# Optimization experiments

Measured on AMD Instinct MI355X. Metric: run time of the kernel, lower is better.

## Reference

```python
import jax, jax.numpy as jnp
from jax import lax
import numpy as np

B, S, D = 64, 512, 256
VOCAB, NC = 50000, 10
N_STEPS = 10  # ode_step=11 points -> 10 intervals, h=0.1
BN_EPS = 1e-5


def setup_inputs() -> dict:
    key = jax.random.key(0)
    ks = jax.random.split(key, 16)
    inp = {}
    inp['input_ids'] = jax.random.randint(ks[0], (B, S), 0, VOCAB)
    inp['emb'] = jax.random.normal(ks[1], (VOCAB, D), dtype=jnp.float32)
    inp['W_ode'] = 0.1 * jax.random.normal(ks[2], (D, D), dtype=jnp.float32)  # init std=0.1
    inp['b_ode'] = jnp.zeros((D,), dtype=jnp.float32)
    for i, kk in enumerate([3, 4, 5]):
        fan_in = D * kk
        inp[f'w{kk}'] = jax.random.normal(ks[3 + 3 * i], (128, D, kk), jnp.float32) / np.sqrt(fan_in)
        inp[f'b{kk}'] = jax.random.normal(ks[4 + 3 * i], (128,), jnp.float32) * 0.01
        inp[f'g{kk}'] = jnp.ones((128,), jnp.float32)
        inp[f'be{kk}'] = jnp.zeros((128,), jnp.float32)
    inp['wc'] = jax.random.normal(ks[12], (NC, D + 3 * 128), jnp.float32) / np.sqrt(D + 3 * 128)
    inp['bc'] = jnp.zeros((NC,), jnp.float32)
    return inp


def _forward(input_ids, emb, W_ode, b_ode, w3, b3, g3, be3, w4, b4, g4, be4,
             w5, b5, g5, be5, wc, bc):
    x = emb[input_ids]                      # (B,S,D)
    # --- Neural ODE branch: linear RHS f(z) = z W^T + b, RK4 fixed-step on [0,1] ---
    z0 = x.reshape(-1, D)                   # (B*S, D)
    h = jnp.float32(1.0 / N_STEPS)

    def f(z):
        return z @ W_ode.T + b_ode

    def step(z, _):
        k1 = f(z)
        k2 = f(z + 0.5 * h * k1)
        k3 = f(z + 0.5 * h * k2)
        k4 = f(z + h * k3)
        return z + (h / 6.0) * (k1 + 2 * k2 + 2 * k3 + k4), None

    z, _ = lax.scan(step, z0, None, length=N_STEPS)
    node_pooled = z.reshape(B, S, D).max(axis=1)   # global max over seq -> (B,D)

    # --- TextCNN branches on raw embeddings ---
    cin = jnp.transpose(x, (0, 2, 1))       # (B,D,S)
    inv_std = jnp.float32(1.0 / np.sqrt(1.0 + BN_EPS))  # BN eval: mean=0, var=1

    def branch(w, b, g, be):
        c = lax.conv_general_dilated(cin, w, (1,), 'VALID',
                                     dimension_numbers=('NCH', 'OIH', 'NCH'))
        c = c + b[None, :, None]
        c = g[None, :, None] * (c * inv_std) + be[None, :, None]
        c = jax.nn.relu(c)
        return c.max(axis=2)                # (B,128)

    p3 = branch(w3, b3, g3, be3)
    p4 = branch(w4, b4, g4, be4)
    p5 = branch(w5, b5, g5, be5)

    feats = jnp.concatenate([node_pooled, p3, p4, p5], axis=1)  # (B,640)
    return feats @ wc.T + bc                # (B,NC); dropout is identity in eval


def reference(input_ids, emb, W_ode, b_ode, w3, b3, g3, be3, w4, b4, g4, be4,
              w5, b5, g5, be5, wc, bc):
    return _forward(input_ids, emb, W_ode, b_ode, w3, b3, g3, be3,
                    w4, b4, g4, be4, w5, b5, g5, be5, wc, bc)
```

## Files before the change

kernel.cpp:

```cpp
#include <hip/hip_runtime.h>


typedef short bf16x8 __attribute__((ext_vector_type(8)));
typedef float f32x4 __attribute__((ext_vector_type(4)));

__device__ __forceinline__ unsigned short f2bf(float f) {
  unsigned u = __float_as_uint(f);
  u += 0x7FFFu + ((u >> 16) & 1u);
  return (unsigned short)(u >> 16);
}

__device__ __forceinline__ float dotcol(const float* __restrict__ xrow,
                                        const float* __restrict__ Y, int tid) {
  float a0 = 0.f, a1 = 0.f, a2 = 0.f, a3 = 0.f;
#pragma unroll 4
  for (int k = 0; k < 256; k += 16) {
    float bv[16];
#pragma unroll
    for (int u = 0; u < 16; ++u) bv[u] = Y[(k + u) * 256 + tid];
#pragma unroll
    for (int u = 0; u < 16; u += 4) {
      a0 = fmaf(xrow[k + u + 0], bv[u + 0], a0);
      a1 = fmaf(xrow[k + u + 1], bv[u + 1], a1);
      a2 = fmaf(xrow[k + u + 2], bv[u + 2], a2);
      a3 = fmaf(xrow[k + u + 3], bv[u + 3], a3);
    }
  }
  return (a0 + a1) + (a2 + a3);
}

__device__ __forceinline__ float rowscan(const float* __restrict__ cvec,
                                         const float* __restrict__ row, float init) {
  float a0 = init, a1 = 0.f, a2 = 0.f, a3 = 0.f;
#pragma unroll 4
  for (int k = 0; k < 256; k += 16) {
    float bv[16];
#pragma unroll
    for (int u = 0; u < 16; ++u) bv[u] = row[k + u];
#pragma unroll
    for (int u = 0; u < 16; u += 4) {
      a0 = fmaf(cvec[k + u + 0], bv[u + 0], a0);
      a1 = fmaf(cvec[k + u + 1], bv[u + 1], a1);
      a2 = fmaf(cvec[k + u + 2], bv[u + 2], a2);
      a3 = fmaf(cvec[k + u + 3], bv[u + 3], a3);
    }
  }
  return (a0 + a1) + (a2 + a3);
}

__global__ __launch_bounds__(256) void k_prep1(
    const float* __restrict__ W, const float* __restrict__ bode,
    const float* __restrict__ w3, const float* __restrict__ w4c, const float* __restrict__ w5,
    float* __restrict__ B, float* __restrict__ c1,
    unsigned short* __restrict__ slab, unsigned* __restrict__ featbuf) {
  __shared__ float r1[256], r2[256], r3[256], red[4];
  const int tid = threadIdx.x, blk = blockIdx.x;
  if (blk < 256) {
    const int i = blk;
    r1[tid] = W[i * 256 + tid];
    __syncthreads();
    const float v2 = dotcol(r1, W, tid);
    r2[tid] = v2;
    __syncthreads();
    const float v3 = dotcol(r2, W, tid);
    r3[tid] = v3;
    __syncthreads();
    const float v4 = dotcol(r3, W, tid);
    const float w1 = r1[tid];
    B[i * 256 + tid] = 0.1f * w1 + 0.005f * v2
                     + (0.001f / 6.f) * v3 + (0.0001f / 24.f) * v4;
    const float q = 0.05f * w1 + (0.01f / 6.f) * v2 + (0.001f / 24.f) * v3;
    float val = bode[tid] * q;
#pragma unroll
    for (int off = 32; off > 0; off >>= 1) val += __shfl_down(val, off);
    if ((tid & 63) == 0) red[tid >> 6] = val;
    __syncthreads();
    if (tid == 0) c1[i] = 0.1f * (bode[i] + ((red[0] + red[1]) + (red[2] + red[3])));
  } else {
    const int base = (blk - 256) * 256 + tid;
#pragma unroll
    for (int u = 0; u < 4; ++u) {
      int e = base + u * 98304;
      int s = e >> 15, r = e & 32767, kd = r >> 7, o = r & 127;
      const float* w; int k, j;
      if (s < 3)      { w = w3;  k = 3; j = s; }
      else if (s < 7) { w = w4c; k = 4; j = s - 3; }
      else            { w = w5;  k = 5; j = s - 7; }
      float val = w[(o * 256 + kd) * k + j];
      int kc = kd >> 5, quad = (kd >> 3) & 3, q8 = kd & 7;
      slab[s * 32768 + ((kc * 4 + quad) * 128 + o) * 8 + q8] = f2bf(val);
    }
    if (base < 64 * 640) featbuf[base] = 0u;
  }
}

__global__ __launch_bounds__(256) void k_prep2(const float* __restrict__ B,
                                               float* __restrict__ N2) {
  __shared__ float xrow[256];
  const int tid = threadIdx.x, i = blockIdx.x;
  xrow[tid] = B[i * 256 + tid];
  __syncthreads();
  const float s = dotcol(xrow, B, tid);
  N2[i * 256 + tid] = ((i == tid) ? 1.f : 0.f) + 2.f * xrow[tid] + s;
}

__global__ __launch_bounds__(256) void k_prep3(
    const float* __restrict__ B, const float* __restrict__ N2,
    const float* __restrict__ c1, float* __restrict__ c10,
    unsigned short* __restrict__ slab) {
  __shared__ float xr[256], c2s[256];
  const int tid = threadIdx.x, blk = blockIdx.x;
  if (blk < 256) {
    xr[tid] = N2[blk * 256 + tid];
    __syncthreads();
    float v = 0.f;
#pragma unroll 1
    for (int it = 0; it < 4; ++it) {
      v = dotcol(xr, N2, tid);
      __syncthreads();
      xr[tid] = v;
      __syncthreads();
    }
    const int o = blk, kd = tid;
    const int kc = kd >> 5, quad = (kd >> 3) & 3, q8 = kd & 7;
    slab[(12 + (o >> 7)) * 32768 + ((kc * 4 + quad) * 128 + (o & 127)) * 8 + q8] = f2bf(v);
  } else {
    const int j = tid;
    xr[tid] = c1[tid];
    __syncthreads();
    float acc = rowscan(xr, B + (size_t)j * 256, 2.f * xr[j]);
    __syncthreads();
    xr[j] = acc; c2s[j] = acc;
    __syncthreads();
#pragma unroll 1
    for (int it = 0; it < 4; ++it) {
      float a = rowscan(xr, N2 + (size_t)j * 256, c2s[j]);
      __syncthreads();
      xr[j] = a;
      __syncthreads();
    }
    c10[j] = xr[j];
  }
}


__global__ __launch_bounds__(256, 2) void k_main(
    const int* __restrict__ ids, const float* __restrict__ emb,
    const unsigned short* __restrict__ slab, const float* __restrict__ ctot,
    const float* __restrict__ b3, const float* __restrict__ g3, const float* __restrict__ be3,
    const float* __restrict__ b4, const float* __restrict__ g4, const float* __restrict__ be4,
    const float* __restrict__ b5, const float* __restrict__ g5, const float* __restrict__ be5,
    unsigned* __restrict__ featbuf) {
  __shared__ alignas(16) unsigned short Xt[68 * 264];
  __shared__ int ids_s[68];
  const int tid = threadIdx.x;
  const int blk = blockIdx.x;
  const int b = blk >> 3;
  const int t0 = (blk & 7) * 64;
  const int lane = tid & 63;
  const int wave = tid >> 6;
  const int m15 = lane & 15;
  const int quad = lane >> 4;

  if (tid < 68) {
    int t = t0 + tid;
    ids_s[tid] = (t < 512) ? ids[b * 512 + t] : -1;
  }
  __syncthreads();
  for (int i = tid; i < 68 * 64; i += 256) {
    int row = i >> 6, s4 = i & 63;
    uint2 v = make_uint2(0u, 0u);
    int id = ids_s[row];
    if (id >= 0) {
      const float4 f = *(const float4*)(emb + (size_t)id * 256 + s4 * 4);
      v.x = (unsigned)f2bf(f.x) | ((unsigned)f2bf(f.y) << 16);
      v.y = (unsigned)f2bf(f.z) | ((unsigned)f2bf(f.w) << 16);
    }
    *(uint2*)&Xt[row * 264 + s4 * 4] = v;
  }
  __syncthreads();

  const unsigned short* fb0 = slab + ((size_t)quad * 128 + (wave * 2 + 0) * 16 + m15) * 8;
  const unsigned short* fb1 = fb0 + 128;

  bf16x8 fA[4], fB[4];
#pragma unroll
  for (int q = 0; q < 4; ++q) {
    fA[q] = *(const bf16x8*)(((q & 1) ? fb1 : fb0) + (q >> 1) * 4096);
    fB[q] = *(const bf16x8*)(((q & 1) ? fb1 : fb0) + 8192 + (q >> 1) * 4096);
  }

  f32x4 acc[4][2];
#pragma unroll
  for (int mt = 0; mt < 4; ++mt)
#pragma unroll
    for (int nt = 0; nt < 2; ++nt) acc[mt][nt] = (f32x4){0.f, 0.f, 0.f, 0.f};

#define ENTRY(KCQ, FR)                                                          \
  {                                                                             \
    _Pragma("unroll")                                                           \
    for (int kc2 = 0; kc2 < 2; ++kc2) {                                         \
      const int kd0 = ((KCQ) * 2 + kc2) * 32 + quad * 8;                        \
      bf16x8 af[4];                                                             \
      _Pragma("unroll")                                                         \
      for (int mt = 0; mt < 4; ++mt)                                            \
        af[mt] = *(const bf16x8*)&Xt[(shift + mt * 16 + m15) * 264 + kd0];      \
      _Pragma("unroll")                                                         \
      for (int mt = 0; mt < 4; ++mt) {                                          \
        acc[mt][0] = __builtin_amdgcn_mfma_f32_16x16x32_bf16(af[mt], FR[kc2 * 2 + 0], acc[mt][0], 0, 0, 0); \
        acc[mt][1] = __builtin_amdgcn_mfma_f32_16x16x32_bf16(af[mt], FR[kc2 * 2 + 1], acc[mt][1], 0, 0, 0); \
      }                                                                         \
    }                                                                           \
  }

  for (int ep = 0; ep < 28; ++ep) {
    const int e0 = ep * 2;
    const int slice = e0 >> 2;
    const int shift = (slice < 3) ? slice
                    : (slice < 7) ? (slice - 3)
                    : (slice < 12) ? (slice - 7) : 0;
    const int kcq0 = e0 & 3;

    ENTRY(kcq0, fA);
    if (ep < 27) {
      const int eo = (e0 + 2) * 8192;
#pragma unroll
      for (int q = 0; q < 4; ++q)
        fA[q] = *(const bf16x8*)(((q & 1) ? fb1 : fb0) + eo + (q >> 1) * 4096);
    }
    ENTRY(kcq0 + 1, fB);
    if (ep < 27) {
      const int eo = (e0 + 3) * 8192;
#pragma unroll
      for (int q = 0; q < 4; ++q)
        fB[q] = *(const bf16x8*)(((q & 1) ? fb1 : fb0) + eo + (q >> 1) * 4096);
    }

    const int g = (ep == 5) ? 0 : (ep == 13) ? 1 : (ep == 23) ? 2
                : (ep == 25) ? 3 : (ep == 27) ? 4 : -1;
    if (g >= 0) {
      if (g < 3) {
        const int kk = g + 3;
        const float* bb  = (g == 0) ? b3 : (g == 1) ? b4 : b5;
        const float* gg  = (g == 0) ? g3 : (g == 1) ? g4 : g5;
        const float* bbe = (g == 0) ? be3 : (g == 1) ? be4 : be5;
        const int off = 256 + g * 128;
        const int tmax = 512 - kk;
#pragma unroll
        for (int nt = 0; nt < 2; ++nt) {
          const int n = (wave * 2 + nt) * 16 + m15;
          const float sc = gg[n] * 0.9999950000375f;
          const float sh = fmaf(sc, bb[n], bbe[n]);
          float mx = 0.f;
#pragma unroll
          for (int mt = 0; mt < 4; ++mt)
#pragma unroll
            for (int r = 0; r < 4; ++r) {
              const int t = t0 + mt * 16 + quad * 4 + r;
              const float v = fmaf(sc, acc[mt][nt][r], sh);
              if (t <= tmax) mx = fmaxf(mx, v);
            }
          mx = fmaxf(mx, __shfl_xor(mx, 16));
          mx = fmaxf(mx, __shfl_xor(mx, 32));
          if (quad == 0) atomicMax(&featbuf[b * 640 + off + n], __float_as_uint(mx));
        }
      } else {
        const int base = (g == 3) ? 0 : 128;
#pragma unroll
        for (int nt = 0; nt < 2; ++nt) {
          const int n = (wave * 2 + nt) * 16 + m15;
          const float ct = ctot[base + n];
          float mx = -3.4e38f;
#pragma unroll
          for (int mt = 0; mt < 4; ++mt)
#pragma unroll
            for (int r = 0; r < 4; ++r)
              mx = fmaxf(mx, acc[mt][nt][r] + ct);
          mx = fmaxf(mx, __shfl_xor(mx, 16));
          mx = fmaxf(mx, __shfl_xor(mx, 32));
          if (quad == 0) {
            unsigned bits = __float_as_uint(mx);
            unsigned key = (bits & 0x80000000u) ? ~bits : (bits | 0x80000000u);
            atomicMax(&featbuf[b * 640 + base + n], key);
          }
        }
      }
#pragma unroll
      for (int mt = 0; mt < 4; ++mt)
#pragma unroll
        for (int nt = 0; nt < 2; ++nt) acc[mt][nt] = (f32x4){0.f, 0.f, 0.f, 0.f};
    }
  }
#undef ENTRY
}

__global__ void k_fin(const unsigned* __restrict__ featbuf, const float* __restrict__ wc,
                      const float* __restrict__ bc, float* __restrict__ out) {
  int b = blockIdx.x, lane = threadIdx.x;
  float p[10];
#pragma unroll
  for (int c = 0; c < 10; ++c) p[c] = 0.f;
  for (int f = lane; f < 640; f += 64) {
    unsigned u = featbuf[b * 640 + f];
    float v;
    if (f < 256) v = (u & 0x80000000u) ? __uint_as_float(u ^ 0x80000000u) : __uint_as_float(~u);
    else v = __uint_as_float(u);
#pragma unroll
    for (int c = 0; c < 10; ++c) p[c] = fmaf(v, wc[c * 640 + f], p[c]);
  }
#pragma unroll
  for (int c = 0; c < 10; ++c) {
    float s = p[c];
#pragma unroll
    for (int off = 32; off > 0; off >>= 1) s += __shfl_down(s, off);
    if (lane == 0) out[b * 10 + c] = s + bc[c];
  }
}

extern "C" void kernel_launch(void* const* d_in, const int* in_sizes, int n_in,
                              void* d_out, int out_size, void* d_ws, size_t ws_size,
                              hipStream_t stream) {
  (void)in_sizes; (void)n_in; (void)out_size; (void)ws_size;
  const int*   ids  = (const int*)d_in[0];
  const float* emb  = (const float*)d_in[1];
  const float* W    = (const float*)d_in[2];
  const float* bode = (const float*)d_in[3];
  const float* w3   = (const float*)d_in[4];
  const float* b3   = (const float*)d_in[5];
  const float* g3   = (const float*)d_in[6];
  const float* be3  = (const float*)d_in[7];
  const float* w4   = (const float*)d_in[8];
  const float* b4   = (const float*)d_in[9];
  const float* g4   = (const float*)d_in[10];
  const float* be4  = (const float*)d_in[11];
  const float* w5   = (const float*)d_in[12];
  const float* b5   = (const float*)d_in[13];
  const float* g5   = (const float*)d_in[14];
  const float* be5  = (const float*)d_in[15];
  const float* wc   = (const float*)d_in[16];
  const float* bc   = (const float*)d_in[17];
  float* out = (float*)d_out;

  float* wsf = (float*)d_ws;
  float* B   = wsf;
  float* N2  = wsf + 65536;
  float* c1  = wsf + 131072;
  float* c10 = wsf + 131328;
  unsigned short* slab = (unsigned short*)(wsf + 131584);
  unsigned* featbuf = (unsigned*)(wsf + 360960);

  hipLaunchKernelGGL(k_prep1, dim3(640), dim3(256), 0, stream,
                     W, bode, w3, w4, w5, B, c1, slab, featbuf);
  hipLaunchKernelGGL(k_prep2, dim3(256), dim3(256), 0, stream, B, N2);
  hipLaunchKernelGGL(k_prep3, dim3(257), dim3(256), 0, stream, B, N2, c1, c10, slab);
  hipLaunchKernelGGL(k_main, dim3(512), dim3(256), 0, stream,
                     ids, emb, slab, c10,
                     b3, g3, be3, b4, g4, be4, b5, g5, be5, featbuf);
  hipLaunchKernelGGL(k_fin, dim3(64), dim3(64), 0, stream, featbuf, wc, bc, out);
}
```

Baseline: 223.2 us.

## Fuse all stages into one persistent kernel with software grid barriers

Merges the three prep kernels, the main conv/ODE kernel and the classifier into a single 512-block launch, separating stages with an atomic-counter grid barrier instead of kernel boundaries. The main loop now keeps four bf16 fragment sets in flight instead of two and issues the fragment loads before the embedding gather. The aim is to remove launch gaps and tail idle time between the five kernels. The risks are a hang if all 512 blocks cannot be co-resident (it relies on 2 blocks per CU), the cost of spinning blocks at each barrier, higher register pressure, and an extra memset launch.

```diff
diff --git a/kernel.cpp b/kernel.cpp
--- a/kernel.cpp
+++ b/kernel.cpp
@@ -48,113 +48,130 @@
   return (a0 + a1) + (a2 + a3);
 }
 
-__global__ __launch_bounds__(256) void k_prep1(
+__device__ __forceinline__ void gbar(unsigned* __restrict__ cnt,
+                                     unsigned* __restrict__ flag) {
+  __syncthreads();
+  if (threadIdx.x == 0) {
+    __threadfence();
+    unsigned my = __hip_atomic_load(flag, __ATOMIC_RELAXED, __HIP_MEMORY_SCOPE_AGENT);
+    if (atomicAdd(cnt, 1u) == 511u) {
+      __hip_atomic_store(cnt, 0u, __ATOMIC_RELAXED, __HIP_MEMORY_SCOPE_AGENT);
+      __hip_atomic_store(flag, my + 1u, __ATOMIC_RELEASE, __HIP_MEMORY_SCOPE_AGENT);
+    } else {
+      while (__hip_atomic_load(flag, __ATOMIC_RELAXED, __HIP_MEMORY_SCOPE_AGENT) == my)
+        __builtin_amdgcn_s_sleep(2);
+    }
+    __threadfence();
+  }
+  __syncthreads();
+}
+
+__global__ __launch_bounds__(256, 2) void k_mega(
+    const int* __restrict__ ids, const float* __restrict__ emb,
     const float* __restrict__ W, const float* __restrict__ bode,
-    const float* __restrict__ w3, const float* __restrict__ w4c, const float* __restrict__ w5,
-    float* __restrict__ B, float* __restrict__ c1,
-    unsigned short* __restrict__ slab, unsigned* __restrict__ featbuf) {
-  __shared__ float r1[256], r2[256], r3[256], red[4];
-  const int tid = threadIdx.x, blk = blockIdx.x;
-  if (blk < 256) {
-    const int i = blk;
-    r1[tid] = W[i * 256 + tid];
-    __syncthreads();
-    const float v2 = dotcol(r1, W, tid);
-    r2[tid] = v2;
-    __syncthreads();
-    const float v3 = dotcol(r2, W, tid);
-    r3[tid] = v3;
-    __syncthreads();
-    const float v4 = dotcol(r3, W, tid);
-    const float w1 = r1[tid];
-    B[i * 256 + tid] = 0.1f * w1 + 0.005f * v2
-                     + (0.001f / 6.f) * v3 + (0.0001f / 24.f) * v4;
-    const float q = 0.05f * w1 + (0.01f / 6.f) * v2 + (0.001f / 24.f) * v3;
-    float val = bode[tid] * q;
-#pragma unroll
-    for (int off = 32; off > 0; off >>= 1) val += __shfl_down(val, off);
-    if ((tid & 63) == 0) red[tid >> 6] = val;
-    __syncthreads();
-    if (tid == 0) c1[i] = 0.1f * (bode[i] + ((red[0] + red[1]) + (red[2] + red[3])));
-  } else {
-    const int base = (blk - 256) * 256 + tid;
-#pragma unroll
-    for (int u = 0; u < 4; ++u) {
-      int e = base + u * 98304;
-      int s = e >> 15, r = e & 32767, kd = r >> 7, o = r & 127;
-      const float* w; int k, j;
-      if (s < 3)      { w = w3;  k = 3; j = s; }
-      else if (s < 7) { w = w4c; k = 4; j = s - 3; }
-      else            { w = w5;  k = 5; j = s - 7; }
-      float val = w[(o * 256 + kd) * k + j];
-      int kc = kd >> 5, quad = (kd >> 3) & 3, q8 = kd & 7;
-      slab[s * 32768 + ((kc * 4 + quad) * 128 + o) * 8 + q8] = f2bf(val);
-    }
-    if (base < 64 * 640) featbuf[base] = 0u;
-  }
-}
-
-__global__ __launch_bounds__(256) void k_prep2(const float* __restrict__ B,
-                                               float* __restrict__ N2) {
-  __shared__ float xrow[256];
-  const int tid = threadIdx.x, i = blockIdx.x;
-  xrow[tid] = B[i * 256 + tid];
-  __syncthreads();
-  const float s = dotcol(xrow, B, tid);
-  N2[i * 256 + tid] = ((i == tid) ? 1.f : 0.f) + 2.f * xrow[tid] + s;
-}
-
-__global__ __launch_bounds__(256) void k_prep3(
-    const float* __restrict__ B, const float* __restrict__ N2,
-    const float* __restrict__ c1, float* __restrict__ c10,
-    unsigned short* __restrict__ slab) {
-  __shared__ float xr[256], c2s[256];
-  const int tid = threadIdx.x, blk = blockIdx.x;
-  if (blk < 256) {
-    xr[tid] = N2[blk * 256 + tid];
-    __syncthreads();
-    float v = 0.f;
-#pragma unroll 1
-    for (int it = 0; it < 4; ++it) {
-      v = dotcol(xr, N2, tid);
-      __syncthreads();
-      xr[tid] = v;
-      __syncthreads();
-    }
-    const int o = blk, kd = tid;
-    const int kc = kd >> 5, quad = (kd >> 3) & 3, q8 = kd & 7;
-    slab[(12 + (o >> 7)) * 32768 + ((kc * 4 + quad) * 128 + (o & 127)) * 8 + q8] = f2bf(v);
-  } else {
-    const int j = tid;
-    xr[tid] = c1[tid];
-    __syncthreads();
-    float acc = rowscan(xr, B + (size_t)j * 256, 2.f * xr[j]);
-    __syncthreads();
-    xr[j] = acc; c2s[j] = acc;
-    __syncthreads();
-#pragma unroll 1
-    for (int it = 0; it < 4; ++it) {
-      float a = rowscan(xr, N2 + (size_t)j * 256, c2s[j]);
-      __syncthreads();
-      xr[j] = a;
-      __syncthreads();
-    }
-    c10[j] = xr[j];
-  }
-}
-
-
-__global__ __launch_bounds__(256, 2) void k_main(
-    const int* __restrict__ ids, const float* __restrict__ emb,
-    const unsigned short* __restrict__ slab, const float* __restrict__ ctot,
-    const float* __restrict__ b3, const float* __restrict__ g3, const float* __restrict__ be3,
-    const float* __restrict__ b4, const float* __restrict__ g4, const float* __restrict__ be4,
-    const float* __restrict__ b5, const float* __restrict__ g5, const float* __restrict__ be5,
-    unsigned* __restrict__ featbuf) {
+    const float* __restrict__ w3c, const float* __restrict__ b3,
+    const float* __restrict__ g3, const float* __restrict__ be3,
+    const float* __restrict__ w4c, const float* __restrict__ b4,
+    const float* __restrict__ g4, const float* __restrict__ be4,
+    const float* __restrict__ w5c, const float* __restrict__ b5,
+    const float* __restrict__ g5, const float* __restrict__ be5,
+    const float* __restrict__ wc, const float* __restrict__ bc,
+    float* __restrict__ out,
+    float* __restrict__ Bm, float* __restrict__ N2,
+    float* __restrict__ c1, float* __restrict__ c10,
+    unsigned short* __restrict__ slab, unsigned* __restrict__ featbuf,
+    unsigned* __restrict__ bar) {
   __shared__ alignas(16) unsigned short Xt[68 * 264];
   __shared__ int ids_s[68];
   const int tid = threadIdx.x;
   const int blk = blockIdx.x;
+
+  float* r1  = (float*)Xt;
+  float* r2  = r1 + 256;
+  float* r3  = r1 + 512;
+  float* red = r1 + 768;
+
+  if (blk < 256) {
+    const int i = blk;
+    r1[tid] = W[i * 256 + tid];
+    __syncthreads();
+    const float v2 = dotcol(r1, W, tid);
+    r2[tid] = v2;
+    __syncthreads();
+    const float v3 = dotcol(r2, W, tid);
+    r3[tid] = v3;
+    __syncthreads();
+    const float v4 = dotcol(r3, W, tid);
+    const float w1 = r1[tid];
+    Bm[i * 256 + tid] = 0.1f * w1 + 0.005f * v2
+                      + (0.001f / 6.f) * v3 + (0.0001f / 24.f) * v4;
+    const float q = 0.05f * w1 + (0.01f / 6.f) * v2 + (0.001f / 24.f) * v3;
+    float val = bode[tid] * q;
+#pragma unroll
+    for (int off = 32; off > 0; off >>= 1) val += __shfl_down(val, off);
+    if ((tid & 63) == 0) red[tid >> 6] = val;
+    __syncthreads();
+    if (tid == 0) c1[i] = 0.1f * (bode[i] + ((red[0] + red[1]) + (red[2] + red[3])));
+  } else {
+    const int base = (blk - 256) * 256 + tid;
+#pragma unroll
+    for (int u = 0; u < 6; ++u) {
+      int e = base + u * 65536;
+      int s = e >> 15, r = e & 32767, kd = r >> 7, o = r & 127;
+      const float* w; int k, j;
+      if (s < 3)      { w = w3c; k = 3; j = s; }
+      else if (s < 7) { w = w4c; k = 4; j = s - 3; }
+      else            { w = w5c; k = 5; j = s - 7; }
+      float val = w[(o * 256 + kd) * k + j];
+      int kc = kd >> 5, quad = (kd >> 3) & 3, q8 = kd & 7;
+      slab[s * 32768 + ((kc * 4 + quad) * 128 + o) * 8 + q8] = f2bf(val);
+    }
+    if (base < 64 * 640) featbuf[base] = 0u;
+  }
+  gbar(bar, bar + 1);
+
+  if (blk < 256) {
+    r1[tid] = Bm[blk * 256 + tid];
+    __syncthreads();
+    const float s = dotcol(r1, Bm, tid);
+    N2[blk * 256 + tid] = ((blk == tid) ? 1.f : 0.f) + 2.f * r1[tid] + s;
+  } else if (blk == 300) {
+    r1[tid] = c1[tid];
+    __syncthreads();
+    const float acc = rowscan(r1, Bm + (size_t)tid * 256, 2.f * r1[tid]);
+    __syncthreads();
+    r1[tid] = acc;
+    r2[tid] = acc;
+    __syncthreads();
+  }
+  gbar(bar, bar + 1);
+
+  if (blk < 256) {
+    r1[tid] = N2[blk * 256 + tid];
+    __syncthreads();
+    float v = 0.f;
+#pragma unroll 1
+    for (int it = 0; it < 4; ++it) {
+      v = dotcol(r1, N2, tid);
+      __syncthreads();
+      r1[tid] = v;
+      __syncthreads();
+    }
+    const int o = blk, kd = tid;
+    const int kc = kd >> 5, quad = (kd >> 3) & 3, q8 = kd & 7;
+    slab[(12 + (o >> 7)) * 32768 + ((kc * 4 + quad) * 128 + (o & 127)) * 8 + q8] = f2bf(v);
+  } else if (blk == 300) {
+#pragma unroll 1
+    for (int it = 0; it < 4; ++it) {
+      const float a = rowscan(r1, N2 + (size_t)tid * 256, r2[tid]);
+      __syncthreads();
+      r1[tid] = a;
+      __syncthreads();
+    }
+    c10[tid] = r1[tid];
+  }
+  gbar(bar, bar + 1);
+
   const int b = blk >> 3;
   const int t0 = (blk & 7) * 64;
   const int lane = tid & 63;
@@ -167,6 +184,19 @@
     ids_s[tid] = (t < 512) ? ids[b * 512 + t] : -1;
   }
   __syncthreads();
+
+  const unsigned short* fb0 = slab + ((size_t)quad * 128 + wave * 2 * 16 + m15) * 8;
+  bf16x8 fA[4], fB[4], fC[4], fD[4];
+#define LDFRAG(DST, EN)                                                         \
+  {                                                                             \
+    const unsigned short* p_ = fb0 + (EN) * 8192;                               \
+    DST[0] = *(const bf16x8*)(p_);                                              \
+    DST[1] = *(const bf16x8*)(p_ + 128);                                        \
+    DST[2] = *(const bf16x8*)(p_ + 4096);                                       \
+    DST[3] = *(const bf16x8*)(p_ + 4096 + 128);                                 \
+  }
+  LDFRAG(fA, 0) LDFRAG(fB, 1) LDFRAG(fC, 2) LDFRAG(fD, 3)
+
   for (int i = tid; i < 68 * 64; i += 256) {
     int row = i >> 6, s4 = i & 63;
     uint2 v = make_uint2(0u, 0u);
@@ -179,16 +209,6 @@
     *(uint2*)&Xt[row * 264 + s4 * 4] = v;
   }
   __syncthreads();
-
-  const unsigned short* fb0 = slab + ((size_t)quad * 128 + (wave * 2 + 0) * 16 + m15) * 8;
-  const unsigned short* fb1 = fb0 + 128;
-
-  bf16x8 fA[4], fB[4];
-#pragma unroll
-  for (int q = 0; q < 4; ++q) {
-    fA[q] = *(const bf16x8*)(((q & 1) ? fb1 : fb0) + (q >> 1) * 4096);
-    fB[q] = *(const bf16x8*)(((q & 1) ? fb1 : fb0) + 8192 + (q >> 1) * 4096);
-  }
 
   f32x4 acc[4][2];
 #pragma unroll
@@ -213,31 +233,16 @@
     }                                                                           \
   }
 
-  for (int ep = 0; ep < 28; ++ep) {
-    const int e0 = ep * 2;
-    const int slice = e0 >> 2;
-    const int shift = (slice < 3) ? slice
-                    : (slice < 7) ? (slice - 3)
-                    : (slice < 12) ? (slice - 7) : 0;
-    const int kcq0 = e0 & 3;
-
-    ENTRY(kcq0, fA);
-    if (ep < 27) {
-      const int eo = (e0 + 2) * 8192;
-#pragma unroll
-      for (int q = 0; q < 4; ++q)
-        fA[q] = *(const bf16x8*)(((q & 1) ? fb1 : fb0) + eo + (q >> 1) * 4096);
-    }
-    ENTRY(kcq0 + 1, fB);
-    if (ep < 27) {
-      const int eo = (e0 + 3) * 8192;
-#pragma unroll
-      for (int q = 0; q < 4; ++q)
-        fB[q] = *(const bf16x8*)(((q & 1) ? fb1 : fb0) + eo + (q >> 1) * 4096);
-    }
-
-    const int g = (ep == 5) ? 0 : (ep == 13) ? 1 : (ep == 23) ? 2
-                : (ep == 25) ? 3 : (ep == 27) ? 4 : -1;
+  for (int eq = 0; eq < 14; ++eq) {
+    const int shift = (eq < 3) ? eq : (eq < 7) ? (eq - 3) : (eq < 12) ? (eq - 7) : 0;
+
+    ENTRY(0, fA) if (eq < 13) LDFRAG(fA, (eq + 1) * 4 + 0)
+    ENTRY(1, fB) if (eq < 13) LDFRAG(fB, (eq + 1) * 4 + 1)
+    ENTRY(2, fC) if (eq < 13) LDFRAG(fC, (eq + 1) * 4 + 2)
+    ENTRY(3, fD) if (eq < 13) LDFRAG(fD, (eq + 1) * 4 + 3)
+
+    const int g = (eq == 2) ? 0 : (eq == 6) ? 1 : (eq == 11) ? 2
+                : (eq == 12) ? 3 : (eq == 13) ? 4 : -1;
     if (g >= 0) {
       if (g < 3) {
         const int kk = g + 3;
@@ -269,7 +274,7 @@
 #pragma unroll
         for (int nt = 0; nt < 2; ++nt) {
           const int n = (wave * 2 + nt) * 16 + m15;
-          const float ct = ctot[base + n];
+          const float ct = c10[base + n];
           float mx = -3.4e38f;
 #pragma unroll
           for (int mt = 0; mt < 4; ++mt)
@@ -292,28 +297,35 @@
     }
   }
 #undef ENTRY
-}
-
-__global__ void k_fin(const unsigned* __restrict__ featbuf, const float* __restrict__ wc,
-                      const float* __restrict__ bc, float* __restrict__ out) {
-  int b = blockIdx.x, lane = threadIdx.x;
-  float p[10];
-#pragma unroll
-  for (int c = 0; c < 10; ++c) p[c] = 0.f;
-  for (int f = lane; f < 640; f += 64) {
-    unsigned u = featbuf[b * 640 + f];
-    float v;
-    if (f < 256) v = (u & 0x80000000u) ? __uint_as_float(u ^ 0x80000000u) : __uint_as_float(~u);
-    else v = __uint_as_float(u);
-#pragma unroll
-    for (int c = 0; c < 10; ++c) p[c] = fmaf(v, wc[c * 640 + f], p[c]);
-  }
-#pragma unroll
-  for (int c = 0; c < 10; ++c) {
-    float s = p[c];
-#pragma unroll
-    for (int off = 32; off > 0; off >>= 1) s += __shfl_down(s, off);
-    if (lane == 0) out[b * 10 + c] = s + bc[c];
+#undef LDFRAG
+
+  gbar(bar, bar + 1);
+  if (blk < 64 && tid < 64) {
+    float vv[10];
+#pragma unroll
+    for (int it = 0; it < 10; ++it) {
+      unsigned u = featbuf[blk * 640 + it * 64 + tid];
+      if (it < 4)
+        vv[it] = (u & 0x80000000u) ? __uint_as_float(u ^ 0x80000000u)
+                                   : __uint_as_float(~u);
+      else
+        vv[it] = __uint_as_float(u);
+    }
+    float p[10];
+#pragma unroll
+    for (int c = 0; c < 10; ++c) p[c] = 0.f;
+#pragma unroll
+    for (int it = 0; it < 10; ++it)
+#pragma unroll
+      for (int c = 0; c < 10; ++c)
+        p[c] = fmaf(vv[it], wc[c * 640 + it * 64 + tid], p[c]);
+#pragma unroll
+    for (int c = 0; c < 10; ++c) {
+      float s = p[c];
+#pragma unroll
+      for (int off = 32; off > 0; off >>= 1) s += __shfl_down(s, off);
+      if (tid == 0) out[blk * 10 + c] = s + bc[c];
+    }
   }
 }
 
@@ -342,19 +354,17 @@
   float* out = (float*)d_out;
 
   float* wsf = (float*)d_ws;
-  float* B   = wsf;
+  float* Bm  = wsf;
   float* N2  = wsf + 65536;
   float* c1  = wsf + 131072;
   float* c10 = wsf + 131328;
   unsigned short* slab = (unsigned short*)(wsf + 131584);
   unsigned* featbuf = (unsigned*)(wsf + 360960);
-
-  hipLaunchKernelGGL(k_prep1, dim3(640), dim3(256), 0, stream,
-                     W, bode, w3, w4, w5, B, c1, slab, featbuf);
-  hipLaunchKernelGGL(k_prep2, dim3(256), dim3(256), 0, stream, B, N2);
-  hipLaunchKernelGGL(k_prep3, dim3(257), dim3(256), 0, stream, B, N2, c1, c10, slab);
-  hipLaunchKernelGGL(k_main, dim3(512), dim3(256), 0, stream,
-                     ids, emb, slab, c10,
-                     b3, g3, be3, b4, g4, be4, b5, g5, be5, featbuf);
-  hipLaunchKernelGGL(k_fin, dim3(64), dim3(64), 0, stream, featbuf, wc, bc, out);
-}
+  unsigned* bar     = (unsigned*)(wsf + 401920);
+
+  hipMemsetAsync(bar, 0, 8, stream);
+  hipLaunchKernelGGL(k_mega, dim3(512), dim3(256), 0, stream,
+                     ids, emb, W, bode,
+                     w3, b3, g3, be3, w4, b4, g4, be4, w5, b5, g5, be5,
+                     wc, bc, out, Bm, N2, c1, c10, slab, featbuf, bar);
+}
```

After: 426.2 us. 1.91x slower.

## Split prep matrix-vector steps across 1024 threads and deepen main fragment prefetch

Applied to the files above, without the earlier changes.

The prep kernels go from 256 to 1024 threads per block. Each row-times-matrix step is split into four K-partitions whose partial sums are reduced through shared memory, and the c-vector recurrence now uses wave-per-row shuffle reductions instead of serial row scans. This is meant to cut the latency of the serial chains of dot products in the prep stage. In the main kernel, weight fragments are now double-buffered four entries deep and loaded before the embedding gather, so more global loads are in flight. That raises register pressure under the existing occupancy-2 launch bound.

```diff
diff --git a/kernel.cpp b/kernel.cpp
--- a/kernel.cpp
+++ b/kernel.cpp
@@ -10,82 +10,67 @@
   return (unsigned short)(u >> 16);
 }
 
-__device__ __forceinline__ float dotcol(const float* __restrict__ xrow,
-                                        const float* __restrict__ Y, int tid) {
+__device__ __forceinline__ void rstep(float* __restrict__ dst, const float* __restrict__ src,
+                                      const float* __restrict__ Y, float* __restrict__ part,
+                                      int t) {
+  const int c = t & 255, g = t >> 8;
+  const float* Yc = Y + (size_t)(g * 64) * 256 + c;
+  const float* sg = src + g * 64;
   float a0 = 0.f, a1 = 0.f, a2 = 0.f, a3 = 0.f;
 #pragma unroll 4
-  for (int k = 0; k < 256; k += 16) {
+  for (int u = 0; u < 64; u += 16) {
     float bv[16];
 #pragma unroll
-    for (int u = 0; u < 16; ++u) bv[u] = Y[(k + u) * 256 + tid];
-#pragma unroll
-    for (int u = 0; u < 16; u += 4) {
-      a0 = fmaf(xrow[k + u + 0], bv[u + 0], a0);
-      a1 = fmaf(xrow[k + u + 1], bv[u + 1], a1);
-      a2 = fmaf(xrow[k + u + 2], bv[u + 2], a2);
-      a3 = fmaf(xrow[k + u + 3], bv[u + 3], a3);
-    }
-  }
-  return (a0 + a1) + (a2 + a3);
-}
-
-__device__ __forceinline__ float rowscan(const float* __restrict__ cvec,
-                                         const float* __restrict__ row, float init) {
-  float a0 = init, a1 = 0.f, a2 = 0.f, a3 = 0.f;
-#pragma unroll 4
-  for (int k = 0; k < 256; k += 16) {
-    float bv[16];
-#pragma unroll
-    for (int u = 0; u < 16; ++u) bv[u] = row[k + u];
-#pragma unroll
-    for (int u = 0; u < 16; u += 4) {
-      a0 = fmaf(cvec[k + u + 0], bv[u + 0], a0);
-      a1 = fmaf(cvec[k + u + 1], bv[u + 1], a1);
-      a2 = fmaf(cvec[k + u + 2], bv[u + 2], a2);
-      a3 = fmaf(cvec[k + u + 3], bv[u + 3], a3);
-    }
-  }
-  return (a0 + a1) + (a2 + a3);
-}
-
-__global__ __launch_bounds__(256) void k_prep1(
+    for (int v = 0; v < 16; ++v) bv[v] = Yc[(u + v) * 256];
+#pragma unroll
+    for (int v = 0; v < 16; v += 4) {
+      a0 = fmaf(sg[u + v + 0], bv[v + 0], a0);
+      a1 = fmaf(sg[u + v + 1], bv[v + 1], a1);
+      a2 = fmaf(sg[u + v + 2], bv[v + 2], a2);
+      a3 = fmaf(sg[u + v + 3], bv[v + 3], a3);
+    }
+  }
+  part[t] = (a0 + a1) + (a2 + a3);
+  __syncthreads();
+  if (t < 256) dst[t] = (part[t] + part[t + 256]) + (part[t + 512] + part[t + 768]);
+  __syncthreads();
+}
+
+__global__ __launch_bounds__(1024) void k_prep1(
     const float* __restrict__ W, const float* __restrict__ bode,
-    const float* __restrict__ w3, const float* __restrict__ w4c, const float* __restrict__ w5,
-    float* __restrict__ B, float* __restrict__ c1,
+    const float* __restrict__ w3c, const float* __restrict__ w4c, const float* __restrict__ w5c,
+    float* __restrict__ Bm, float* __restrict__ c1,
     unsigned short* __restrict__ slab, unsigned* __restrict__ featbuf) {
-  __shared__ float r1[256], r2[256], r3[256], red[4];
-  const int tid = threadIdx.x, blk = blockIdx.x;
+  __shared__ float part[1024], ra[256], rb[256], rc[256], rd[256], red[4];
+  const int t = threadIdx.x, blk = blockIdx.x;
   if (blk < 256) {
     const int i = blk;
-    r1[tid] = W[i * 256 + tid];
+    if (t < 256) ra[t] = W[i * 256 + t];
     __syncthreads();
-    const float v2 = dotcol(r1, W, tid);
-    r2[tid] = v2;
+    rstep(rb, ra, W, part, t);
+    rstep(rc, rb, W, part, t);
+    rstep(rd, rc, W, part, t);
+    if (t < 256) {
+      Bm[i * 256 + t] = 0.1f * ra[t] + 0.005f * rb[t]
+                      + (0.001f / 6.f) * rc[t] + (0.0001f / 24.f) * rd[t];
+      const float q = 0.05f * ra[t] + (0.01f / 6.f) * rb[t] + (0.001f / 24.f) * rc[t];
+      float val = bode[t] * q;
+#pragma unroll
+      for (int off = 32; off > 0; off >>= 1) val += __shfl_down(val, off);
+      if ((t & 63) == 0) red[t >> 6] = val;
+    }
     __syncthreads();
-    const float v3 = dotcol(r2, W, tid);
-    r3[tid] = v3;
-    __syncthreads();
-    const float v4 = dotcol(r3, W, tid);
-    const float w1 = r1[tid];
-    B[i * 256 + tid] = 0.1f * w1 + 0.005f * v2
-                     + (0.001f / 6.f) * v3 + (0.0001f / 24.f) * v4;
-    const float q = 0.05f * w1 + (0.01f / 6.f) * v2 + (0.001f / 24.f) * v3;
-    float val = bode[tid] * q;
-#pragma unroll
-    for (int off = 32; off > 0; off >>= 1) val += __shfl_down(val, off);
-    if ((tid & 63) == 0) red[tid >> 6] = val;
-    __syncthreads();
-    if (tid == 0) c1[i] = 0.1f * (bode[i] + ((red[0] + red[1]) + (red[2] + red[3])));
+    if (t == 0) c1[i] = 0.1f * (bode[i] + ((red[0] + red[1]) + (red[2] + red[3])));
   } else {
-    const int base = (blk - 256) * 256 + tid;
+    const int base = (blk - 256) * 1024 + t;
 #pragma unroll
     for (int u = 0; u < 4; ++u) {
       int e = base + u * 98304;
       int s = e >> 15, r = e & 32767, kd = r >> 7, o = r & 127;
       const float* w; int k, j;
-      if (s < 3)      { w = w3;  k = 3; j = s; }
+      if (s < 3)      { w = w3c; k = 3; j = s; }
       else if (s < 7) { w = w4c; k = 4; j = s - 3; }
-      else            { w = w5;  k = 5; j = s - 7; }
+      else            { w = w5c; k = 5; j = s - 7; }
       float val = w[(o * 256 + kd) * k + j];
       int kc = kd >> 5, quad = (kd >> 3) & 3, q8 = kd & 7;
       slab[s * 32768 + ((kc * 4 + quad) * 128 + o) * 8 + q8] = f2bf(val);
@@ -94,52 +79,68 @@
   }
 }
 
-__global__ __launch_bounds__(256) void k_prep2(const float* __restrict__ B,
-                                               float* __restrict__ N2) {
-  __shared__ float xrow[256];
-  const int tid = threadIdx.x, i = blockIdx.x;
-  xrow[tid] = B[i * 256 + tid];
-  __syncthreads();
-  const float s = dotcol(xrow, B, tid);
-  N2[i * 256 + tid] = ((i == tid) ? 1.f : 0.f) + 2.f * xrow[tid] + s;
-}
-
-__global__ __launch_bounds__(256) void k_prep3(
-    const float* __restrict__ B, const float* __restrict__ N2,
+__global__ __launch_bounds__(1024) void k_prep2(const float* __restrict__ Bm,
+                                                float* __restrict__ N2) {
+  __shared__ float part[1024], ra[256], rb[256];
+  const int t = threadIdx.x, i = blockIdx.x;
+  if (t < 256) ra[t] = Bm[i * 256 + t];
+  __syncthreads();
+  rstep(rb, ra, Bm, part, t);
+  if (t < 256) N2[i * 256 + t] = ((i == t) ? 1.f : 0.f) + 2.f * ra[t] + rb[t];
+}
+
+__global__ __launch_bounds__(1024) void k_prep3(
+    const float* __restrict__ Bm, const float* __restrict__ N2,
     const float* __restrict__ c1, float* __restrict__ c10,
     unsigned short* __restrict__ slab) {
-  __shared__ float xr[256], c2s[256];
-  const int tid = threadIdx.x, blk = blockIdx.x;
+  __shared__ float part[1024], ra[256], rb[256], rc[256], rd[256];
+  const int t = threadIdx.x, blk = blockIdx.x;
   if (blk < 256) {
-    xr[tid] = N2[blk * 256 + tid];
+    if (t < 256) ra[t] = N2[blk * 256 + t];
     __syncthreads();
-    float v = 0.f;
-#pragma unroll 1
-    for (int it = 0; it < 4; ++it) {
-      v = dotcol(xr, N2, tid);
-      __syncthreads();
-      xr[tid] = v;
-      __syncthreads();
-    }
-    const int o = blk, kd = tid;
-    const int kc = kd >> 5, quad = (kd >> 3) & 3, q8 = kd & 7;
-    slab[(12 + (o >> 7)) * 32768 + ((kc * 4 + quad) * 128 + (o & 127)) * 8 + q8] = f2bf(v);
+    rstep(ra, ra, N2, part, t);
+    rstep(ra, ra, N2, part, t);
+    rstep(ra, ra, N2, part, t);
+    rstep(ra, ra, N2, part, t);
+    if (t < 256) {
+      const int o = blk, kd = t;
+      const int kc = kd >> 5, quad = (kd >> 3) & 3, q8 = kd & 7;
+      slab[(12 + (o >> 7)) * 32768 + ((kc * 4 + quad) * 128 + (o & 127)) * 8 + q8] = f2bf(ra[t]);
+    }
   } else {
-    const int j = tid;
-    xr[tid] = c1[tid];
+    const int w = t >> 6, lane = t & 63;
+    if (t < 256) { ra[t] = c1[t]; rd[t] = 2.f * c1[t]; }
     __syncthreads();
-    float acc = rowscan(xr, B + (size_t)j * 256, 2.f * xr[j]);
-    __syncthreads();
-    xr[j] = acc; c2s[j] = acc;
-    __syncthreads();
-#pragma unroll 1
-    for (int it = 0; it < 4; ++it) {
-      float a = rowscan(xr, N2 + (size_t)j * 256, c2s[j]);
-      __syncthreads();
-      xr[j] = a;
-      __syncthreads();
-    }
-    c10[j] = xr[j];
+#define CSTEP(SRC, YMAT, ADD2, DST)                                             \
+    {                                                                           \
+      for (int r0i = 0; r0i < 16; r0i += 4) {                                   \
+        float bv[4][4];                                                         \
+        _Pragma("unroll")                                                       \
+        for (int rr = 0; rr < 4; ++rr) {                                        \
+          const int j = w * 16 + r0i + rr;                                      \
+          _Pragma("unroll")                                                     \
+          for (int q = 0; q < 4; ++q) bv[rr][q] = YMAT[j * 256 + lane + 64 * q];\
+        }                                                                       \
+        _Pragma("unroll")                                                       \
+        for (int rr = 0; rr < 4; ++rr) {                                        \
+          const int j = w * 16 + r0i + rr;                                      \
+          float v = 0.f;                                                        \
+          _Pragma("unroll")                                                     \
+          for (int q = 0; q < 4; ++q) v = fmaf(SRC[lane + 64 * q], bv[rr][q], v);\
+          _Pragma("unroll")                                                     \
+          for (int off = 32; off > 0; off >>= 1) v += __shfl_down(v, off);      \
+          if (lane == 0) DST[j] = ADD2[j] + v;                                  \
+        }                                                                       \
+      }                                                                         \
+      __syncthreads();                                                          \
+    }
+    CSTEP(ra, Bm, rd, rb)
+    CSTEP(rb, N2, rb, rc)
+    CSTEP(rc, N2, rb, rd)
+    CSTEP(rd, N2, rb, rc)
+    CSTEP(rc, N2, rb, rd)
+#undef CSTEP
+    if (t < 256) c10[t] = rd[t];
   }
 }
 
@@ -167,6 +168,19 @@
     ids_s[tid] = (t < 512) ? ids[b * 512 + t] : -1;
   }
   __syncthreads();
+
+  const unsigned short* fb0 = slab + ((size_t)quad * 128 + wave * 2 * 16 + m15) * 8;
+  bf16x8 fA[4], fB[4], fC[4], fD[4];
+#define LDFRAG(DST, EN)                                                         \
+  {                                                                             \
+    const unsigned short* p_ = fb0 + (EN) * 8192;                               \
+    DST[0] = *(const bf16x8*)(p_);                                              \
+    DST[1] = *(const bf16x8*)(p_ + 128);                                        \
+    DST[2] = *(const bf16x8*)(p_ + 4096);                                       \
+    DST[3] = *(const bf16x8*)(p_ + 4096 + 128);                                 \
+  }
+  LDFRAG(fA, 0) LDFRAG(fB, 1) LDFRAG(fC, 2) LDFRAG(fD, 3)
+
   for (int i = tid; i < 68 * 64; i += 256) {
     int row = i >> 6, s4 = i & 63;
     uint2 v = make_uint2(0u, 0u);
@@ -179,16 +193,6 @@
     *(uint2*)&Xt[row * 264 + s4 * 4] = v;
   }
   __syncthreads();
-
-  const unsigned short* fb0 = slab + ((size_t)quad * 128 + (wave * 2 + 0) * 16 + m15) * 8;
-  const unsigned short* fb1 = fb0 + 128;
-
-  bf16x8 fA[4], fB[4];
-#pragma unroll
-  for (int q = 0; q < 4; ++q) {
-    fA[q] = *(const bf16x8*)(((q & 1) ? fb1 : fb0) + (q >> 1) * 4096);
-    fB[q] = *(const bf16x8*)(((q & 1) ? fb1 : fb0) + 8192 + (q >> 1) * 4096);
-  }
 
   f32x4 acc[4][2];
 #pragma unroll
@@ -213,31 +217,16 @@
     }                                                                           \
   }
 
-  for (int ep = 0; ep < 28; ++ep) {
-    const int e0 = ep * 2;
-    const int slice = e0 >> 2;
-    const int shift = (slice < 3) ? slice
-                    : (slice < 7) ? (slice - 3)
-                    : (slice < 12) ? (slice - 7) : 0;
-    const int kcq0 = e0 & 3;
-
-    ENTRY(kcq0, fA);
-    if (ep < 27) {
-      const int eo = (e0 + 2) * 8192;
-#pragma unroll
-      for (int q = 0; q < 4; ++q)
-        fA[q] = *(const bf16x8*)(((q & 1) ? fb1 : fb0) + eo + (q >> 1) * 4096);
-    }
-    ENTRY(kcq0 + 1, fB);
-    if (ep < 27) {
-      const int eo = (e0 + 3) * 8192;
-#pragma unroll
-      for (int q = 0; q < 4; ++q)
-        fB[q] = *(const bf16x8*)(((q & 1) ? fb1 : fb0) + eo + (q >> 1) * 4096);
-    }
-
-    const int g = (ep == 5) ? 0 : (ep == 13) ? 1 : (ep == 23) ? 2
-                : (ep == 25) ? 3 : (ep == 27) ? 4 : -1;
+  for (int eq = 0; eq < 14; ++eq) {
+    const int shift = (eq < 3) ? eq : (eq < 7) ? (eq - 3) : (eq < 12) ? (eq - 7) : 0;
+
+    ENTRY(0, fA) if (eq < 13) LDFRAG(fA, (eq + 1) * 4 + 0)
+    ENTRY(1, fB) if (eq < 13) LDFRAG(fB, (eq + 1) * 4 + 1)
+    ENTRY(2, fC) if (eq < 13) LDFRAG(fC, (eq + 1) * 4 + 2)
+    ENTRY(3, fD) if (eq < 13) LDFRAG(fD, (eq + 1) * 4 + 3)
+
+    const int g = (eq == 2) ? 0 : (eq == 6) ? 1 : (eq == 11) ? 2
+                : (eq == 12) ? 3 : (eq == 13) ? 4 : -1;
     if (g >= 0) {
       if (g < 3) {
         const int kk = g + 3;
@@ -292,6 +281,7 @@
     }
   }
 #undef ENTRY
+#undef LDFRAG
 }
 
 __global__ void k_fin(const unsigned* __restrict__ featbuf, const float* __restrict__ wc,
@@ -342,17 +332,17 @@
   float* out = (float*)d_out;
 
   float* wsf = (float*)d_ws;
-  float* B   = wsf;
+  float* Bm  = wsf;
   float* N2  = wsf + 65536;
   float* c1  = wsf + 131072;
   float* c10 = wsf + 131328;
   unsigned short* slab = (unsigned short*)(wsf + 131584);
   unsigned* featbuf = (unsigned*)(wsf + 360960);
 
-  hipLaunchKernelGGL(k_prep1, dim3(640), dim3(256), 0, stream,
-                     W, bode, w3, w4, w5, B, c1, slab, featbuf);
-  hipLaunchKernelGGL(k_prep2, dim3(256), dim3(256), 0, stream, B, N2);
-  hipLaunchKernelGGL(k_prep3, dim3(257), dim3(256), 0, stream, B, N2, c1, c10, slab);
+  hipLaunchKernelGGL(k_prep1, dim3(352), dim3(1024), 0, stream,
+                     W, bode, w3, w4, w5, Bm, c1, slab, featbuf);
+  hipLaunchKernelGGL(k_prep2, dim3(256), dim3(1024), 0, stream, Bm, N2);
+  hipLaunchKernelGGL(k_prep3, dim3(257), dim3(1024), 0, stream, Bm, N2, c1, c10, slab);
   hipLaunchKernelGGL(k_main, dim3(512), dim3(256), 0, stream,
                      ids, emb, slab, c10,
                      b3, g3, be3, b4, g4, be4, b5, g5, be5, featbuf);
```

New measurement: 242.7 us. 1.09x slower.

## Replace repeated squaring with binomial expansion of (I+B)^10 in one prep kernel

Applied to the files above, without the earlier changes.

The old prep computed N2=(I+B)^2 and then squared it repeatedly in a second kernel, with a separate block for the bias vector. The new code expands (I+B)^10 as a binomial sum of powers B^k: each block computes one row through nine successive vector-matrix products and accumulates the bias term with block reductions along the way. This removes one kernel launch and the N2 buffer. The cost is nine dependent matvecs per row instead of five, and dotcol is restructured to issue 64 loads per batch with the outer loop not unrolled.

```diff
diff --git a/kernel.cpp b/kernel.cpp
--- a/kernel.cpp
+++ b/kernel.cpp
@@ -10,39 +10,20 @@
   return (unsigned short)(u >> 16);
 }
 
-__device__ __forceinline__ float dotcol(const float* __restrict__ xrow,
-                                        const float* __restrict__ Y, int tid) {
+__device__ __forceinline__ float dotcol64(const float* __restrict__ xrow,
+                                          const float* __restrict__ Y, int c) {
   float a0 = 0.f, a1 = 0.f, a2 = 0.f, a3 = 0.f;
-#pragma unroll 4
-  for (int k = 0; k < 256; k += 16) {
-    float bv[16];
-#pragma unroll
-    for (int u = 0; u < 16; ++u) bv[u] = Y[(k + u) * 256 + tid];
-#pragma unroll
-    for (int u = 0; u < 16; u += 4) {
-      a0 = fmaf(xrow[k + u + 0], bv[u + 0], a0);
-      a1 = fmaf(xrow[k + u + 1], bv[u + 1], a1);
-      a2 = fmaf(xrow[k + u + 2], bv[u + 2], a2);
-      a3 = fmaf(xrow[k + u + 3], bv[u + 3], a3);
-    }
-  }
-  return (a0 + a1) + (a2 + a3);
-}
-
-__device__ __forceinline__ float rowscan(const float* __restrict__ cvec,
-                                         const float* __restrict__ row, float init) {
-  float a0 = init, a1 = 0.f, a2 = 0.f, a3 = 0.f;
-#pragma unroll 4
-  for (int k = 0; k < 256; k += 16) {
-    float bv[16];
-#pragma unroll
-    for (int u = 0; u < 16; ++u) bv[u] = row[k + u];
-#pragma unroll
-    for (int u = 0; u < 16; u += 4) {
-      a0 = fmaf(cvec[k + u + 0], bv[u + 0], a0);
-      a1 = fmaf(cvec[k + u + 1], bv[u + 1], a1);
-      a2 = fmaf(cvec[k + u + 2], bv[u + 2], a2);
-      a3 = fmaf(cvec[k + u + 3], bv[u + 3], a3);
+#pragma unroll 1
+  for (int w = 0; w < 4; ++w) {
+    float bv[64];
+#pragma unroll
+    for (int v = 0; v < 64; ++v) bv[v] = Y[(w * 64 + v) * 256 + c];
+#pragma unroll
+    for (int v = 0; v < 64; v += 4) {
+      a0 = fmaf(xrow[w * 64 + v + 0], bv[v + 0], a0);
+      a1 = fmaf(xrow[w * 64 + v + 1], bv[v + 1], a1);
+      a2 = fmaf(xrow[w * 64 + v + 2], bv[v + 2], a2);
+      a3 = fmaf(xrow[w * 64 + v + 3], bv[v + 3], a3);
     }
   }
   return (a0 + a1) + (a2 + a3);
@@ -50,8 +31,8 @@
 
 __global__ __launch_bounds__(256) void k_prep1(
     const float* __restrict__ W, const float* __restrict__ bode,
-    const float* __restrict__ w3, const float* __restrict__ w4c, const float* __restrict__ w5,
-    float* __restrict__ B, float* __restrict__ c1,
+    const float* __restrict__ w3c, const float* __restrict__ w4c, const float* __restrict__ w5c,
+    float* __restrict__ Bm, float* __restrict__ c1,
     unsigned short* __restrict__ slab, unsigned* __restrict__ featbuf) {
   __shared__ float r1[256], r2[256], r3[256], red[4];
   const int tid = threadIdx.x, blk = blockIdx.x;
@@ -59,16 +40,16 @@
     const int i = blk;
     r1[tid] = W[i * 256 + tid];
     __syncthreads();
-    const float v2 = dotcol(r1, W, tid);
+    const float v2 = dotcol64(r1, W, tid);
     r2[tid] = v2;
     __syncthreads();
-    const float v3 = dotcol(r2, W, tid);
+    const float v3 = dotcol64(r2, W, tid);
     r3[tid] = v3;
     __syncthreads();
-    const float v4 = dotcol(r3, W, tid);
+    const float v4 = dotcol64(r3, W, tid);
     const float w1 = r1[tid];
-    B[i * 256 + tid] = 0.1f * w1 + 0.005f * v2
-                     + (0.001f / 6.f) * v3 + (0.0001f / 24.f) * v4;
+    Bm[i * 256 + tid] = 0.1f * w1 + 0.005f * v2
+                      + (0.001f / 6.f) * v3 + (0.0001f / 24.f) * v4;
     const float q = 0.05f * w1 + (0.01f / 6.f) * v2 + (0.001f / 24.f) * v3;
     float val = bode[tid] * q;
 #pragma unroll
@@ -83,9 +64,9 @@
       int e = base + u * 98304;
       int s = e >> 15, r = e & 32767, kd = r >> 7, o = r & 127;
       const float* w; int k, j;
-      if (s < 3)      { w = w3;  k = 3; j = s; }
+      if (s < 3)      { w = w3c; k = 3; j = s; }
       else if (s < 7) { w = w4c; k = 4; j = s - 3; }
-      else            { w = w5;  k = 5; j = s - 7; }
+      else            { w = w5c; k = 5; j = s - 7; }
       float val = w[(o * 256 + kd) * k + j];
       int kc = kd >> 5, quad = (kd >> 3) & 3, q8 = kd & 7;
       slab[s * 32768 + ((kc * 4 + quad) * 128 + o) * 8 + q8] = f2bf(val);
@@ -94,53 +75,46 @@
   }
 }
 
-__global__ __launch_bounds__(256) void k_prep2(const float* __restrict__ B,
-                                               float* __restrict__ N2) {
-  __shared__ float xrow[256];
+__global__ __launch_bounds__(256) void k_prep2(
+    const float* __restrict__ Bm, const float* __restrict__ c1v,
+    float* __restrict__ c10, unsigned short* __restrict__ slab) {
+  __shared__ float curs[256], c1s[256], red[4];
   const int tid = threadIdx.x, i = blockIdx.x;
-  xrow[tid] = B[i * 256 + tid];
+  const float coefN[11] = {1.f, 10.f, 45.f, 120.f, 210.f, 252.f,
+                           210.f, 120.f, 45.f, 10.f, 1.f};
+  float v = Bm[i * 256 + tid];
+  curs[tid] = v;
+  c1s[tid] = c1v[tid];
+  float n10 = ((i == tid) ? 1.f : 0.f) + 10.f * v;
+  float pd = v * c1s[tid];
+#pragma unroll
+  for (int off = 32; off > 0; off >>= 1) pd += __shfl_down(pd, off);
+  if ((tid & 63) == 0) red[tid >> 6] = pd;
   __syncthreads();
-  const float s = dotcol(xrow, B, tid);
-  N2[i * 256 + tid] = ((i == tid) ? 1.f : 0.f) + 2.f * xrow[tid] + s;
-}
-
-__global__ __launch_bounds__(256) void k_prep3(
-    const float* __restrict__ B, const float* __restrict__ N2,
-    const float* __restrict__ c1, float* __restrict__ c10,
-    unsigned short* __restrict__ slab) {
-  __shared__ float xr[256], c2s[256];
-  const int tid = threadIdx.x, blk = blockIdx.x;
-  if (blk < 256) {
-    xr[tid] = N2[blk * 256 + tid];
-    __syncthreads();
-    float v = 0.f;
+  float ct = 10.f * c1s[i] + 45.f * ((red[0] + red[1]) + (red[2] + red[3]));
+
 #pragma unroll 1
-    for (int it = 0; it < 4; ++it) {
-      v = dotcol(xr, N2, tid);
-      __syncthreads();
-      xr[tid] = v;
-      __syncthreads();
-    }
-    const int o = blk, kd = tid;
+  for (int k = 2; k <= 10; ++k) {
+    v = dotcol64(curs, Bm, tid);
+    n10 = fmaf(coefN[k], v, n10);
+    float pdk = v * c1s[tid];
+#pragma unroll
+    for (int off = 32; off > 0; off >>= 1) pdk += __shfl_down(pdk, off);
+    if ((tid & 63) == 0) red[tid >> 6] = pdk;
+    __syncthreads();
+    if (k <= 9) {
+      ct = fmaf(coefN[k + 1], (red[0] + red[1]) + (red[2] + red[3]), ct);
+    }
+    curs[tid] = v;
+    __syncthreads();
+  }
+
+  {
+    const int o = i, kd = tid;
     const int kc = kd >> 5, quad = (kd >> 3) & 3, q8 = kd & 7;
-    slab[(12 + (o >> 7)) * 32768 + ((kc * 4 + quad) * 128 + (o & 127)) * 8 + q8] = f2bf(v);
-  } else {
-    const int j = tid;
-    xr[tid] = c1[tid];
-    __syncthreads();
-    float acc = rowscan(xr, B + (size_t)j * 256, 2.f * xr[j]);
-    __syncthreads();
-    xr[j] = acc; c2s[j] = acc;
-    __syncthreads();
-#pragma unroll 1
-    for (int it = 0; it < 4; ++it) {
-      float a = rowscan(xr, N2 + (size_t)j * 256, c2s[j]);
-      __syncthreads();
-      xr[j] = a;
-      __syncthreads();
-    }
-    c10[j] = xr[j];
-  }
+    slab[(12 + (o >> 7)) * 32768 + ((kc * 4 + quad) * 128 + (o & 127)) * 8 + q8] = f2bf(n10);
+  }
+  if (tid == 0) c10[i] = ct;
 }
 
 
@@ -342,17 +316,15 @@
   float* out = (float*)d_out;
 
   float* wsf = (float*)d_ws;
-  float* B   = wsf;
-  float* N2  = wsf + 65536;
-  float* c1  = wsf + 131072;
-  float* c10 = wsf + 131328;
-  unsigned short* slab = (unsigned short*)(wsf + 131584);
-  unsigned* featbuf = (unsigned*)(wsf + 360960);
+  float* Bm  = wsf;
+  float* c1  = wsf + 65536;
+  float* c10 = wsf + 65792;
+  unsigned short* slab = (unsigned short*)(wsf + 66048);
+  unsigned* featbuf = (unsigned*)(wsf + 295424);
 
   hipLaunchKernelGGL(k_prep1, dim3(640), dim3(256), 0, stream,
-                     W, bode, w3, w4, w5, B, c1, slab, featbuf);
-  hipLaunchKernelGGL(k_prep2, dim3(256), dim3(256), 0, stream, B, N2);
-  hipLaunchKernelGGL(k_prep3, dim3(257), dim3(256), 0, stream, B, N2, c1, c10, slab);
+                     W, bode, w3, w4, w5, Bm, c1, slab, featbuf);
+  hipLaunchKernelGGL(k_prep2, dim3(256), dim3(256), 0, stream, Bm, c1, c10, slab);
   hipLaunchKernelGGL(k_main, dim3(512), dim3(256), 0, stream,
                      ids, emb, slab, c10,
                      b3, g3, be3, b4, g4, be4, b5, g5, be5, featbuf);
```

Result: faster. 200.1 us (-10.4%).
